# Kernel optimization log

Hardware: AMD Instinct MI355X
Metric: run time of the kernel (lower is better)

Reference implementation:

```python
import jax, jax.numpy as jnp
import numpy as np

NUM_HEADS = 16
NEG_INF = -1e9


def setup_inputs() -> dict:
    key = jax.random.key(0)
    ks = jax.random.split(key, 12)
    T, B, E = 2048, 4, 1024
    s = 0.02
    inp = {
        "query": jax.random.normal(ks[0], (T, B, E), jnp.float32),
        "key": jax.random.normal(ks[1], (T, B, E), jnp.float32),
        "value": jax.random.normal(ks[2], (T, B, E), jnp.float32),
        # causal additive mask [T, S]: 0 on/below diagonal, -1e9 above
        "attn_mask": jnp.where(
            jnp.arange(T)[:, None] >= jnp.arange(T)[None, :], 0.0, NEG_INF
        ).astype(jnp.float32),
        "wq": jax.random.normal(ks[3], (E, E), jnp.float32) * s,
        "bq": jax.random.normal(ks[4], (E,), jnp.float32) * s,
        "wk": jax.random.normal(ks[5], (E, E), jnp.float32) * s,
        "bk": jax.random.normal(ks[6], (E,), jnp.float32) * s,
        "wv": jax.random.normal(ks[7], (E, E), jnp.float32) * s,
        "bv": jax.random.normal(ks[8], (E,), jnp.float32) * s,
        "wo": jax.random.normal(ks[9], (E, E), jnp.float32) * s,
        "bo": jax.random.normal(ks[10], (E,), jnp.float32) * s,
    }
    return inp


def reference(query, key, value, attn_mask, wq, bq, wk, bk, wv, bv, wo, bo):
    T, B, E = query.shape
    H = NUM_HEADS
    D = E // H
    scaling = D ** (-0.5)
    # projections (torch Linear: x @ W.T + b)
    q = (query @ wq.T + bq) * scaling          # [T, B, E]
    k = key @ wk.T + bk                         # [S, B, E]
    v = value @ wv.T + bv                       # [S, B, E]
    # -> [B*H, len, D]
    q = q.reshape(T, B * H, D).transpose(1, 0, 2)
    k = k.reshape(-1, B * H, D).transpose(1, 0, 2)
    v = v.reshape(-1, B * H, D).transpose(1, 0, 2)
    # scores [B*H, T, S], additive mask, softmax (dropout = identity in eval)
    attn_weights = jnp.einsum('ntd,nsd->nts', q, k) + attn_mask
    attn_weights = jax.nn.softmax(attn_weights, axis=-1)
    attn = jnp.einsum('nts,nsd->ntd', attn_weights, v)   # [B*H, T, D]
    attn = attn.transpose(1, 0, 2).reshape(T, B, E)
    return attn @ wo.T + bo
```

## Files before the change

kernel.cpp:

```cpp
#include <hip/hip_runtime.h>
#include <hip/hip_bf16.h>

typedef __hip_bfloat16 bf16;
typedef __attribute__((ext_vector_type(8))) short short8;
typedef __attribute__((ext_vector_type(4))) float float4v;
typedef __attribute__((ext_vector_type(2))) unsigned long long ull2;
typedef __attribute__((ext_vector_type(2))) unsigned int uint2v;

#define TLEN  2048
#define BATCH 4
#define EMB   1024
#define HEADS 16
#define HD    64
#define MROWS (TLEN*BATCH)
#define PSTRIDE 72
#define SMAX2 5.770780f
#define QSCALE 0.18033688f

#if __has_builtin(__builtin_amdgcn_exp2f)
#define EXP2(x) __builtin_amdgcn_exp2f(x)
#else
#define EXP2(x) exp2f(x)
#endif

__device__ __forceinline__ unsigned pack_bf16_2(float lo, float hi) {
    unsigned a = __float_as_uint(lo) + 0x8000u;
    unsigned b = __float_as_uint(hi) + 0x8000u;
#if __has_builtin(__builtin_amdgcn_perm)
    return __builtin_amdgcn_perm(b, a, 0x07060302u);
#else
    return (a >> 16) | (b & 0xFFFF0000u);
#endif
}

__device__ __forceinline__ void gl2lds16(const bf16* g, bf16* l) {
    __builtin_amdgcn_global_load_lds(
        (const __attribute__((address_space(1))) void*)g,
        (__attribute__((address_space(3))) void*)l, 16, 0, 0);
}

__device__ __forceinline__ void store_out(float* p, float v)  { *p = v; }
__device__ __forceinline__ void store_out(bf16* p, float v)   { *p = __float2bfloat16(v); }

__device__ __forceinline__ void cvt8(const float* __restrict__ src,
                                     bf16* __restrict__ dst, int t) {
    const float4v a = ((const float4v*)src)[2*t];
    const float4v b = ((const float4v*)src)[2*t + 1];
    union { short8 v; bf16 h[8]; } u;
    u.h[0] = __float2bfloat16(a[0]);
    u.h[1] = __float2bfloat16(a[1]);
    u.h[2] = __float2bfloat16(a[2]);
    u.h[3] = __float2bfloat16(a[3]);
    u.h[4] = __float2bfloat16(b[0]);
    u.h[5] = __float2bfloat16(b[1]);
    u.h[6] = __float2bfloat16(b[2]);
    u.h[7] = __float2bfloat16(b[3]);
    ((short8*)dst)[t] = u.v;
}

__global__ __launch_bounds__(256)
void cvt_all(const float* __restrict__ q, const float* __restrict__ k,
             const float* __restrict__ v,
             const float* __restrict__ wq, const float* __restrict__ wk,
             const float* __restrict__ wv, const float* __restrict__ wo,
             bf16* __restrict__ xq, bf16* __restrict__ xk, bf16* __restrict__ xv,
             bf16* __restrict__ wqb, bf16* __restrict__ wkb,
             bf16* __restrict__ wvb, bf16* __restrict__ wob)
{
    const int id = blockIdx.x * 256 + threadIdx.x;
    const int NA = 1 << 20, NW = 1 << 17;
    if (id < 3*NA) {
        const int w = id >> 20, off = id & (NA - 1);
        const float* s = w == 0 ? q : (w == 1 ? k : v);
        bf16*        d = w == 0 ? xq : (w == 1 ? xk : xv);
        cvt8(s, d, off);
    } else {
        const int id2 = id - 3*NA;
        const int w = id2 >> 17, off = id2 & (NW - 1);
        const float* s = w == 0 ? wq : (w == 1 ? wk : (w == 2 ? wv : wo));
        bf16*        d = w == 0 ? wqb : (w == 1 ? wkb : (w == 2 ? wvb : wob));
        cvt8(s, d, off);
    }
}

template<typename OutT>
__device__ __forceinline__ void gemm_body(
    const bf16* __restrict__ A, const bf16* __restrict__ Bw,
    const float* __restrict__ bias, OutT* __restrict__ out,
    float scale, int mode, int bm, int bn)
{
    __shared__ __align__(16) bf16 smem[128*64*2];
    bf16* As = smem;
    bf16* Bs = smem + 128*64;
    const int tid  = threadIdx.x;
    const int lane = tid & 63;
    const int wave = tid >> 6;
    const int wm   = (wave >> 1) * 64;
    const int wn   = (wave & 1) * 64;
    const int quad = lane >> 4;
    const int l16  = lane & 15;
    const int hl   = wn >> 6;

    const int srow = tid >> 3;
    const int skc  = (tid & 7) ^ (srow & 7);
    const bf16* Ag = A  + (size_t)(bm*128 + srow)*EMB + skc*8;
    const bf16* Bg = Bw + (size_t)(bn*128 + srow)*EMB + skc*8;
    bf16* Al = As + tid*8;
    bf16* Bl = Bs + tid*8;

    float4v acc[4][4];
    #pragma unroll
    for (int i=0;i<4;i++)
        #pragma unroll
        for (int j=0;j<4;j++) acc[i][j] = (float4v){0.f,0.f,0.f,0.f};

    for (int k0 = 0; k0 < EMB; k0 += 64) {
        __syncthreads();
        #pragma unroll
        for (int g=0; g<4; g++) {
            gl2lds16(Ag + (size_t)g*32*EMB + k0, Al + g*2048);
            gl2lds16(Bg + (size_t)g*32*EMB + k0, Bl + g*2048);
        }
        __syncthreads();

        #pragma unroll
        for (int half=0; half<2; half++) {
            const int pc = (((half<<2) | quad) ^ (l16 & 7)) * 8;
            short8 af[4], bfr[4];
            #pragma unroll
            for (int i=0;i<4;i++)
                af[i] = *(const short8*)(As + (wm + i*16 + l16)*64 + pc);
            #pragma unroll
            for (int j=0;j<4;j++)
                bfr[j] = *(const short8*)(Bs + (wn + j*16 + l16)*64 + pc);
            #pragma unroll
            for (int i=0;i<4;i++)
                #pragma unroll
                for (int j=0;j<4;j++)
                    acc[i][j] = __builtin_amdgcn_mfma_f32_16x16x32_bf16(
                                    af[i], bfr[j], acc[i][j], 0, 0, 0);
        }
    }

    if (mode != 2) {
        #pragma unroll
        for (int i=0;i<4;i++) {
            #pragma unroll
            for (int j=0;j<4;j++) {
                const int n = bn*128 + wn + j*16 + l16;
                const float bf = bias[n];
                #pragma unroll
                for (int r=0;r<4;r++) {
                    const int m = bm*128 + wm + i*16 + quad*4 + r;
                    const float v = (acc[i][j][r] + bf) * scale;
                    size_t idx;
                    if (mode == 0) {
                        idx = (size_t)m*EMB + n;
                    } else {
                        const int t = m >> 2, b = m & 3;
                        const int h = n >> 6, d = n & 63;
                        idx = (((size_t)(b*HEADS + h))*TLEN + t)*HD + d;
                    }
                    store_out(out + idx, v);
                }
            }
        }
    } else {
        __syncthreads();
        bf16* Tb = smem;
        #pragma unroll
        for (int i=0;i<4;i++) {
            const int tc = (wm >> 4) + i;
            #pragma unroll
            for (int j=0;j<4;j++) {
                const int d = j*16 + l16;
                const float bf = bias[bn*128 + wn + d];
                #pragma unroll
                for (int r=0;r<4;r++) {
                    const float v = acc[i][j][r] + bf;
                    Tb[((((r<<1)|hl)*64 + d) << 5) + ((tc ^ (d & 7)) << 2) + quad]
                        = __float2bfloat16(v);
                }
            }
        }
        __syncthreads();
        bf16* ob = (bf16*)out;
        #pragma unroll
        for (int pass=0; pass<8; pass++) {
            const int row = pass*64 + (tid >> 2);
            const int c16 = tid & 3;
            const int b2  = row >> 7;
            const int h2l = (row >> 6) & 1;
            const int d   = row & 63;
            const int e   = d & 7;
            const unsigned long long lo =
                *(const unsigned long long*)(Tb + (row << 5) + ((( (2*c16)   ^ e) << 2)));
            const unsigned long long hi =
                *(const unsigned long long*)(Tb + (row << 5) + ((( (2*c16+1) ^ e) << 2)));
            ull2 val; val.x = lo; val.y = hi;
            *(ull2*)(ob + ((size_t)((b2*HEADS + bn*2 + h2l)*HD + d))*TLEN
                        + bm*32 + c16*8) = val;
        }
    }
}

__global__ __launch_bounds__(256, 2)
void gemm_qkv(const bf16* __restrict__ xq, const bf16* __restrict__ xk,
              const bf16* __restrict__ xv,
              const bf16* __restrict__ wq, const bf16* __restrict__ wk,
              const bf16* __restrict__ wv,
              const float* __restrict__ bq, const float* __restrict__ bk,
              const float* __restrict__ bv,
              bf16* __restrict__ oq, bf16* __restrict__ ok,
              bf16* __restrict__ ov)
{
    const int id  = blockIdx.x;
    const int xcd = id & 7;
    const int r   = id >> 3;
    const int z   = r >> 6;
    const int rem = r & 63;
    const int bm  = xcd + 8*(rem >> 3);
    const int bn  = rem & 7;

    const bf16*  A  = z == 0 ? xq : (z == 1 ? xk : xv);
    const bf16*  W  = z == 0 ? wq : (z == 1 ? wk : wv);
    const float* bi = z == 0 ? bq : (z == 1 ? bk : bv);
    bf16*        o  = z == 0 ? oq : (z == 1 ? ok : ov);
    const float  sc = z == 0 ? QSCALE : 1.0f;
    const int    md = z == 2 ? 2 : 1;
    gemm_body<bf16>(A, W, bi, o, sc, md, bm, bn);
}

__global__ __launch_bounds__(256, 2)
void gemm_out(const bf16* __restrict__ A, const bf16* __restrict__ W,
              const float* __restrict__ bias, float* __restrict__ out)
{
    const int id  = blockIdx.x;
    const int xcd = id & 7;
    const int r   = id >> 3;
    const int bm  = xcd + 8*(r >> 3);
    const int bn  = r & 7;
    gemm_body<float>(A, W, bias, out, 1.0f, 0, bm, bn);
}

__global__ __launch_bounds__(256, 2)
void flash_attn(const bf16* __restrict__ Q, const bf16* __restrict__ K,
                const bf16* __restrict__ Vt, bf16* __restrict__ Aout)
{
    __shared__ __align__(16) bf16 Ks[2][64*64];
    __shared__ __align__(16) bf16 Vs[2][64*64];
    __shared__ __align__(16) bf16 Ps[4*32*PSTRIDE];
    const int tid  = threadIdx.x;
    const int lane = tid & 63;
    const int wave = tid >> 6;
    const int quad = lane >> 4;
    const int l16  = lane & 15;

    const int id  = blockIdx.x;
    const int xcd = id & 7;
    const int jj  = id >> 3;
    const int bh  = xcd + 8*(jj & 7);
    const int tq  = 15 - (jj >> 3);
    const int qbase = tq*128 + wave*32;

    short8 qf[2][2];
    #pragma unroll
    for (int f=0; f<2; f++) {
        const bf16* qrow = Q + ((size_t)bh*TLEN + qbase + f*16 + l16)*HD;
        qf[f][0] = *(const short8*)(qrow + quad*8);
        qf[f][1] = *(const short8*)(qrow + 32 + quad*8);
    }

    float4v o[2][4];
    float lsum[2] = {0.f, 0.f};
    #pragma unroll
    for (int f=0; f<2; f++)
        #pragma unroll
        for (int j=0;j<4;j++) { o[f][j] = (float4v){0.f,0.f,0.f,0.f}; }

    bf16* Pw = Ps + wave*32*PSTRIDE;

    const int srow   = tid >> 3;
    const int schunk = (tid & 7) ^ (srow & 7);
    const bf16* Kg = K  + (size_t)bh*TLEN*HD + (size_t)srow*HD   + schunk*8;
    const bf16* Vg = Vt + (size_t)bh*HD*TLEN + (size_t)srow*TLEN + schunk*8;
    const int ldst = tid*8;

    const int nt = 2*tq + 2;
    gl2lds16(Kg,           &Ks[0][ldst]);
    gl2lds16(Kg + 32*HD,   &Ks[0][32*64 + ldst]);
    gl2lds16(Vg,           &Vs[0][ldst]);
    gl2lds16(Vg + 32*TLEN, &Vs[0][32*64 + ldst]);

    for (int i = 0; i < nt; i++) {
        const int buf = i & 1;
        __syncthreads();
        if (i + 1 < nt) {
            const int nb = buf ^ 1;
            const size_t s0n = (size_t)(i+1)*64;
            gl2lds16(Kg + s0n*HD,        &Ks[nb][ldst]);
            gl2lds16(Kg + (s0n+32)*HD,   &Ks[nb][32*64 + ldst]);
            gl2lds16(Vg + s0n,           &Vs[nb][ldst]);
            gl2lds16(Vg + 32*TLEN + s0n, &Vs[nb][32*64 + ldst]);
        }

        float4v scr[2][4];
        #pragma unroll
        for (int f=0; f<2; f++)
            #pragma unroll
            for (int j=0;j<4;j++)
                scr[f][j] = (float4v){-SMAX2,-SMAX2,-SMAX2,-SMAX2};
        #pragma unroll
        for (int h2=0; h2<2; h2++) {
            const int psw = ((h2<<2) | quad) ^ (l16 & 7);
            #pragma unroll
            for (int j=0;j<4;j++) {
                short8 kf = *(const short8*)(&Ks[buf][(j*16 + l16)*64 + psw*8]);
                scr[0][j] = __builtin_amdgcn_mfma_f32_16x16x32_bf16(kf, qf[0][h2], scr[0][j], 0,0,0);
                scr[1][j] = __builtin_amdgcn_mfma_f32_16x16x32_bf16(kf, qf[1][h2], scr[1][j], 0,0,0);
            }
        }

        #pragma unroll
        for (int f=0; f<2; f++) {
            const int t = qbase + f*16 + l16;
            const bool needmask = (i*64 + 63) > (qbase + f*16);
            #pragma unroll
            for (int j=0;j<4;j++) {
                float p0, p1, p2, p3;
                if (needmask) {
                    const int s = i*64 + j*16 + quad*4;
                    p0 = (s   <= t) ? EXP2(scr[f][j][0]) : 0.f;
                    p1 = (s+1 <= t) ? EXP2(scr[f][j][1]) : 0.f;
                    p2 = (s+2 <= t) ? EXP2(scr[f][j][2]) : 0.f;
                    p3 = (s+3 <= t) ? EXP2(scr[f][j][3]) : 0.f;
                } else {
                    p0 = EXP2(scr[f][j][0]);
                    p1 = EXP2(scr[f][j][1]);
                    p2 = EXP2(scr[f][j][2]);
                    p3 = EXP2(scr[f][j][3]);
                }
                lsum[f] += (p0 + p1) + (p2 + p3);
                uint2v w;
                w.x = pack_bf16_2(p0, p1);
                w.y = pack_bf16_2(p2, p3);
                *(uint2v*)(Pw + (f*16 + l16)*PSTRIDE + j*16 + quad*4) = w;
            }
        }

        #pragma unroll
        for (int h2=0; h2<2; h2++) {
            const int psw = ((h2<<2) | quad) ^ (l16 & 7);
            short8 pf0 = *(const short8*)(Pw + (l16)*PSTRIDE      + h2*32 + quad*8);
            short8 pf1 = *(const short8*)(Pw + (16 + l16)*PSTRIDE + h2*32 + quad*8);
            #pragma unroll
            for (int j=0;j<4;j++) {
                short8 vf = *(const short8*)(&Vs[buf][(j*16 + l16)*64 + psw*8]);
                o[0][j] = __builtin_amdgcn_mfma_f32_16x16x32_bf16(pf0, vf, o[0][j], 0,0,0);
                o[1][j] = __builtin_amdgcn_mfma_f32_16x16x32_bf16(pf1, vf, o[1][j], 0,0,0);
            }
        }
    }

    const int b = bh >> 4, h = bh & 15;
    #pragma unroll
    for (int f=0; f<2; f++) {
        float s = lsum[f];
        s += __shfl_xor(s, 16);
        s += __shfl_xor(s, 32);
        float rn[4];
        #pragma unroll
        for (int r=0;r<4;r++)
            rn[r] = 1.0f / __shfl(s, quad*4 + r, 16);
        #pragma unroll
        for (int j=0;j<4;j++)
            #pragma unroll
            for (int r=0;r<4;r++) {
                const int t = qbase + f*16 + quad*4 + r;
                const int d = j*16 + l16;
                Aout[((size_t)t*BATCH + b)*EMB + h*64 + d] =
                    __float2bfloat16(o[f][j][r] * rn[r]);
            }
    }
}

extern "C" void kernel_launch(void* const* d_in, const int* in_sizes, int n_in,
                              void* d_out, int out_size, void* d_ws, size_t ws_size,
                              hipStream_t stream)
{
    const float* query = (const float*)d_in[0];
    const float* key   = (const float*)d_in[1];
    const float* value = (const float*)d_in[2];
    const float* wq = (const float*)d_in[4];
    const float* bq = (const float*)d_in[5];
    const float* wk = (const float*)d_in[6];
    const float* bk = (const float*)d_in[7];
    const float* wv = (const float*)d_in[8];
    const float* bv = (const float*)d_in[9];
    const float* wo = (const float*)d_in[10];
    const float* bo = (const float*)d_in[11];

    const size_t actsz = (size_t)MROWS*EMB;
    const size_t wsz   = (size_t)EMB*EMB;
    bf16* xq    = (bf16*)d_ws;
    bf16* xk    = xq  + actsz;
    bf16* xv    = xk  + actsz;
    bf16* wqb   = xv  + actsz;
    bf16* wkb   = wqb + wsz;
    bf16* wvb   = wkb + wsz;
    bf16* wob   = wvb + wsz;
    bf16* q_ws  = wob + wsz;
    bf16* k_ws  = q_ws + actsz;
    bf16* v_ws  = k_ws + actsz;

    const dim3 blk(256);

    hipLaunchKernelGGL(cvt_all, dim3(14336), blk, 0, stream,
                       query, key, value, wq, wk, wv, wo,
                       xq, xk, xv, wqb, wkb, wvb, wob);

    hipLaunchKernelGGL(gemm_qkv, dim3(1536), blk, 0, stream,
                       xq, xk, xv, wqb, wkb, wvb, bq, bk, bv, q_ws, k_ws, v_ws);

    hipLaunchKernelGGL(flash_attn, dim3(1024), blk, 0, stream, q_ws, k_ws, v_ws, xq);

    hipLaunchKernelGGL(gemm_out, dim3(512), blk, 0, stream, xq, wob, bo, (float*)d_out);
}
```

Measured before the change: 291.5 us.

## Skip fully masked tiles per wave, compute row sums via MFMA, use packed cvt

Each wave now skips the QK, softmax and PV work for key tiles that lie entirely above its causal diagonal, while still taking part in the shared loads and barriers. The softmax row-sum is computed by an extra MFMA against a vector of ones, replacing the scalar adds and the end-of-kernel shuffle reduction. The manual bf16 packing is replaced by the hardware v_cvt_pk_bf16_f32 instruction, and s_setprio raises wave priority around the MFMA sections. The sum is now taken from bf16-rounded probabilities, which shifts precision slightly, and the MFMA and cvt paths add a small amount of instruction work.

```diff
diff --git a/kernel.cpp b/kernel.cpp
--- a/kernel.cpp
+++ b/kernel.cpp
@@ -23,14 +23,10 @@
 #define EXP2(x) exp2f(x)
 #endif
 
-__device__ __forceinline__ unsigned pack_bf16_2(float lo, float hi) {
-    unsigned a = __float_as_uint(lo) + 0x8000u;
-    unsigned b = __float_as_uint(hi) + 0x8000u;
-#if __has_builtin(__builtin_amdgcn_perm)
-    return __builtin_amdgcn_perm(b, a, 0x07060302u);
-#else
-    return (a >> 16) | (b & 0xFFFF0000u);
-#endif
+__device__ __forceinline__ unsigned cvt_pk_bf16(float lo, float hi) {
+    unsigned r;
+    asm("v_cvt_pk_bf16_f32 %0, %1, %2" : "=v"(r) : "v"(lo), "v"(hi));
+    return r;
 }
 
 __device__ __forceinline__ void gl2lds16(const bf16* g, bf16* l) {
@@ -271,12 +267,19 @@
         qf[f][1] = *(const short8*)(qrow + 32 + quad*8);
     }
 
+    union { short8 v; short h[8]; } onesu;
+    #pragma unroll
+    for (int z=0; z<8; z++) onesu.h[z] = (short)0x3F80;
+    const short8 ones8 = onesu.v;
+
     float4v o[2][4];
-    float lsum[2] = {0.f, 0.f};
+    float4v lsacc[2];
     #pragma unroll
-    for (int f=0; f<2; f++)
+    for (int f=0; f<2; f++) {
+        lsacc[f] = (float4v){0.f,0.f,0.f,0.f};
         #pragma unroll
         for (int j=0;j<4;j++) { o[f][j] = (float4v){0.f,0.f,0.f,0.f}; }
+    }
 
     bf16* Pw = Ps + wave*32*PSTRIDE;
 
@@ -304,12 +307,16 @@
             gl2lds16(Vg + 32*TLEN + s0n, &Vs[nb][32*64 + ldst]);
         }
 
+        const bool live = (i*64) <= (qbase + 31);
+        if (live) {
+
         float4v scr[2][4];
         #pragma unroll
         for (int f=0; f<2; f++)
             #pragma unroll
             for (int j=0;j<4;j++)
                 scr[f][j] = (float4v){-SMAX2,-SMAX2,-SMAX2,-SMAX2};
+        __builtin_amdgcn_s_setprio(1);
         #pragma unroll
         for (int h2=0; h2<2; h2++) {
             const int psw = ((h2<<2) | quad) ^ (l16 & 7);
@@ -320,6 +327,7 @@
                 scr[1][j] = __builtin_amdgcn_mfma_f32_16x16x32_bf16(kf, qf[1][h2], scr[1][j], 0,0,0);
             }
         }
+        __builtin_amdgcn_s_setprio(0);
 
         #pragma unroll
         for (int f=0; f<2; f++) {
@@ -340,19 +348,21 @@
                     p2 = EXP2(scr[f][j][2]);
                     p3 = EXP2(scr[f][j][3]);
                 }
-                lsum[f] += (p0 + p1) + (p2 + p3);
                 uint2v w;
-                w.x = pack_bf16_2(p0, p1);
-                w.y = pack_bf16_2(p2, p3);
+                w.x = cvt_pk_bf16(p0, p1);
+                w.y = cvt_pk_bf16(p2, p3);
                 *(uint2v*)(Pw + (f*16 + l16)*PSTRIDE + j*16 + quad*4) = w;
             }
         }
 
+        __builtin_amdgcn_s_setprio(1);
         #pragma unroll
         for (int h2=0; h2<2; h2++) {
             const int psw = ((h2<<2) | quad) ^ (l16 & 7);
             short8 pf0 = *(const short8*)(Pw + (l16)*PSTRIDE      + h2*32 + quad*8);
             short8 pf1 = *(const short8*)(Pw + (16 + l16)*PSTRIDE + h2*32 + quad*8);
+            lsacc[0] = __builtin_amdgcn_mfma_f32_16x16x32_bf16(pf0, ones8, lsacc[0], 0,0,0);
+            lsacc[1] = __builtin_amdgcn_mfma_f32_16x16x32_bf16(pf1, ones8, lsacc[1], 0,0,0);
             #pragma unroll
             for (int j=0;j<4;j++) {
                 short8 vf = *(const short8*)(&Vs[buf][(j*16 + l16)*64 + psw*8]);
@@ -360,18 +370,18 @@
                 o[1][j] = __builtin_amdgcn_mfma_f32_16x16x32_bf16(pf1, vf, o[1][j], 0,0,0);
             }
         }
+        __builtin_amdgcn_s_setprio(0);
+
+        }
     }
 
     const int b = bh >> 4, h = bh & 15;
     #pragma unroll
     for (int f=0; f<2; f++) {
-        float s = lsum[f];
-        s += __shfl_xor(s, 16);
-        s += __shfl_xor(s, 32);
         float rn[4];
         #pragma unroll
         for (int r=0;r<4;r++)
-            rn[r] = 1.0f / __shfl(s, quad*4 + r, 16);
+            rn[r] = 1.0f / lsacc[f][r];
         #pragma unroll
         for (int j=0;j<4;j++)
             #pragma unroll
```

Result: slower. 299.9 us, median of 2 (+2.9%).
